# Kernel optimization log

Measured on AMD Instinct MI355X. Metric: run time of the kernel, lower is better.

The kernel has to match this reference:

```python
import jax, jax.numpy as jnp
import numpy as np
from jax import lax

# dims (see shape_source)
B, C, H, W = 2, 128, 48, 48
HEADS = 4
G = 4                 # offset_groups = heads
DH = C // HEADS       # 32, dim_head
DF = 4                # downsample_factor
OKS = 6               # offset_kernel_size
PAD = (OKS - DF) // 2 # 1
OFFSET_SCALE = 4.0
CPB_DIM = C // 4      # 32
OD = C // G           # offset_dims = 32


def setup_inputs() -> dict:
    key = jax.random.key(0)
    ks = jax.random.split(key, 12)
    rn = lambda k, shape, s=0.05: jax.random.normal(k, shape, dtype=jnp.float32) * s
    return {
        "x": jax.random.normal(ks[0], (B, C, H, W), dtype=jnp.float32),
        "gamma": jax.random.normal(ks[1], (1,), dtype=jnp.float32),  # nn.Parameter([0.0]); randomized so both paths contribute
        "wq": rn(ks[2], (G, DH, C // G)),    # grouped 1x1 conv, groups=G
        "wk": rn(ks[3], (G, DH, C // G)),
        "wv": rn(ks[4], (G, DH, C // G)),
        "wo": rn(ks[5], (C, C)),             # to_out 1x1 conv
        "bo": jnp.zeros((C,), jnp.float32),
        "w_off_dw": rn(ks[6], (OD, 1, OKS, OKS)),  # depthwise conv k=6 s=4 p=1
        "b_off_dw": jnp.zeros((OD,), jnp.float32),
        "w_off_proj": rn(ks[7], (2, OD)),          # 1x1 conv to 2 offset channels, no bias
        "cpb_w0": rn(ks[8], (2, CPB_DIM), 0.5),
        "cpb_b0": jnp.zeros((CPB_DIM,), jnp.float32),
        "cpb_w1": rn(ks[9], (CPB_DIM, CPB_DIM), 0.2),
        "cpb_b1": jnp.zeros((CPB_DIM,), jnp.float32),
        "cpb_w2": rn(ks[10], (CPB_DIM, HEADS // G), 0.2),
        "cpb_b2": jnp.zeros((HEADS // G,), jnp.float32),
    }


def _bilinear_sample(img, px, py):
    """F.grid_sample(mode='bilinear', padding_mode='zeros') on pixel coords.
    img: (N, Cg, Hi, Wi); px, py: (N, Ho, Wo) -> (N, Cg, Ho, Wo)"""
    N, Cg, Hi, Wi = img.shape
    imgf = img.reshape(N, Cg, Hi * Wi)
    x0 = jnp.floor(px)
    y0 = jnp.floor(py)
    wx1 = px - x0
    wy1 = py - y0

    def corner(xc, yc, w):
        valid = (xc >= 0) & (xc <= Wi - 1) & (yc >= 0) & (yc <= Hi - 1)
        xi = jnp.clip(xc, 0, Wi - 1).astype(jnp.int32)
        yi = jnp.clip(yc, 0, Hi - 1).astype(jnp.int32)
        idx = (yi * Wi + xi).reshape(N, -1)
        vals = jnp.take_along_axis(imgf, idx[:, None, :], axis=2)  # (N,Cg,Ho*Wo)
        return vals * (w * valid).reshape(N, 1, -1)

    out = (corner(x0, y0, (1 - wx1) * (1 - wy1))
           + corner(x0 + 1, y0, wx1 * (1 - wy1))
           + corner(x0, y0 + 1, (1 - wx1) * wy1)
           + corner(x0 + 1, y0 + 1, wx1 * wy1))
    return out.reshape(N, Cg, px.shape[1], px.shape[2])


def _forward(x, gamma, wq, wk, wv, wo, bo, w_off_dw, b_off_dw, w_off_proj,
             cpb_w0, cpb_b0, cpb_w1, cpb_b1, cpb_w2, cpb_b2):
    b = x.shape[0]
    scale = DH ** -0.5
    xg = x.reshape(b, G, C // G, H, W)
    # grouped 1x1 conv -> queries (b, G, DH, H, W); channel layout (g d) == (h d) since G==HEADS
    q = jnp.einsum('bgchw,goc->bgohw', xg, wq)
    gq = q.reshape(b * G, DH, H, W)
    # to_offsets: depthwise conv (k=6, s=4, p=1) -> GELU -> 1x1 to 2ch -> tanh -> *offset_scale
    off = lax.conv_general_dilated(gq, w_off_dw, (DF, DF), [(PAD, PAD), (PAD, PAD)],
                                   feature_group_count=OD,
                                   dimension_numbers=('NCHW', 'OIHW', 'NCHW'))
    off = jax.nn.gelu(off + b_off_dw[None, :, None, None], approximate=False)
    off = jnp.tanh(jnp.einsum('bchw,oc->bohw', off, w_off_proj)) * OFFSET_SCALE  # (bG,2,Hd,Wd)
    Hd, Wd = off.shape[-2], off.shape[-1]
    gy, gx = jnp.meshgrid(jnp.arange(Hd, dtype=jnp.float32),
                          jnp.arange(Wd, dtype=jnp.float32), indexing='ij')
    vg0 = gx[None] + off[:, 0]  # channel 0 = x (meshgrid 'xy' in torch code)
    vg1 = gy[None] + off[:, 1]  # channel 1 = y
    vn0 = 2.0 * vg0 / max(Hd - 1, 1) - 1.0  # normalize_grid (H==W so h/w quirk is moot)
    vn1 = 2.0 * vg1 / max(Wd - 1, 1) - 1.0
    # grid_sample align_corners=False unnormalization: pix = ((u+1)*size - 1)/2
    px = ((vn0 + 1.0) * W - 1.0) / 2.0
    py = ((vn1 + 1.0) * H - 1.0) / 2.0
    kv = _bilinear_sample(xg.reshape(b * G, C // G, H, W), px, py)  # (bG, C/G, Hd, Wd)
    kvg = kv.reshape(b, G, C // G, Hd, Wd)
    k = jnp.einsum('bgchw,goc->bgohw', kvg, wk)
    v = jnp.einsum('bgchw,goc->bgohw', kvg, wv)
    i, j = H * W, Hd * Wd
    qh = q.reshape(b, HEADS, DH, i).transpose(0, 1, 3, 2) * scale  # (b,h,i,d)
    kh = k.reshape(b, HEADS, DH, j).transpose(0, 1, 3, 2)
    vh = v.reshape(b, HEADS, DH, j).transpose(0, 1, 3, 2)
    sim = jnp.einsum('bhid,bhjd->bhij', qh, kh)
    # CPB relative position bias
    gyq, gxq = jnp.meshgrid(jnp.arange(H, dtype=jnp.float32),
                            jnp.arange(W, dtype=jnp.float32), indexing='ij')
    qn0 = 2.0 * gxq / max(H - 1, 1) - 1.0
    qn1 = 2.0 * gyq / max(W - 1, 1) - 1.0
    grid_q = jnp.stack([qn0, qn1], -1).reshape(1, i, 1, 2)
    grid_kv = jnp.stack([vn0, vn1], -1).reshape(b * G, 1, j, 2)
    pos = grid_q - grid_kv                       # (bG, i, j, 2)
    bias = jnp.sign(pos) * jnp.log1p(jnp.abs(pos))
    h1 = jax.nn.relu(bias @ cpb_w0 + cpb_b0)
    h2 = jax.nn.relu(h1 @ cpb_w1 + cpb_b1)
    bias = h2 @ cpb_w2 + cpb_b2                  # (bG, i, j, heads//G)
    bias = bias.reshape(b, G, i, j, HEADS // G).transpose(0, 1, 4, 2, 3).reshape(b, HEADS, i, j)
    attn = jax.nn.softmax(sim + bias, axis=-1)
    outh = jnp.einsum('bhij,bhjd->bhid', attn, vh)
    out = outh.transpose(0, 1, 3, 2).reshape(b, C, H, W)  # 'b h (x y) d -> b (h d) x y'
    attention = jnp.einsum('bchw,oc->bohw', out, wo) + bo[None, :, None, None]
    return gamma[0] * attention + x, attention


def reference(x, gamma, wq, wk, wv, wo, bo, w_off_dw, b_off_dw, w_off_proj,
              cpb_w0, cpb_b0, cpb_w1, cpb_b1, cpb_w2, cpb_b2):
    return _forward(x, gamma, wq, wk, wv, wo, bo, w_off_dw, b_off_dw, w_off_proj,
                    cpb_w0, cpb_b0, cpb_w1, cpb_b1, cpb_w2, cpb_b2)
```

## Files before the change

### kernel.cpp

```cpp
#include <hip/hip_runtime.h>
#include <math.h>

#define HWHW 2304
#define JD   144
#define LSP  148

typedef __attribute__((ext_vector_type(8))) short short8;
typedef __attribute__((ext_vector_type(4))) float f32x4;

__device__ inline ushort f2bf(float f) {
  uint u = __float_as_uint(f);
  u += 0x7fffu + ((u >> 16) & 1u);
  return (ushort)(u >> 16);
}
__device__ inline float bf2f(ushort s) { return __uint_as_float((uint)s << 16); }


__global__ __launch_bounds__(256) void qproj_kernel(
    const float* __restrict__ x, const float* __restrict__ wq,
    ushort* __restrict__ qt) {
  int hw = blockIdx.x * 256 + threadIdx.x;
  int o0 = blockIdx.y * 8, bg = blockIdx.z;
  int b = bg >> 2, g = bg & 3;
  const float* xp = x + (b * 128 + g * 32) * HWHW + hw;
  float xv[32];
#pragma unroll
  for (int c = 0; c < 32; ++c) xv[c] = xp[c * HWHW];
  uint p[4];
#pragma unroll
  for (int oo = 0; oo < 8; oo += 2) {
    const float* w0r = wq + (g * 32 + o0 + oo) * 32;
    const float* w1r = wq + (g * 32 + o0 + oo + 1) * 32;
    float a0 = 0.f, a1 = 0.f;
#pragma unroll
    for (int c = 0; c < 32; ++c) { a0 += w0r[c] * xv[c]; a1 += w1r[c] * xv[c]; }
    p[oo >> 1] = (uint)f2bf(a0) | ((uint)f2bf(a1) << 16);
  }
  *(uint4*)(qt + ((long)bg * HWHW + hw) * 32 + o0) = make_uint4(p[0], p[1], p[2], p[3]);
}

__global__ __launch_bounds__(384) void offset_kv_kernel(
    const ushort* __restrict__ qt, const float* __restrict__ wdw,
    const float* __restrict__ bdw, const float* __restrict__ wproj,
    const float* __restrict__ x, const float* __restrict__ wk,
    const float* __restrict__ wv,
    float* __restrict__ vn0, float* __restrict__ vn1,
    ushort* __restrict__ ktb, ushort* __restrict__ vtb) {
  __shared__ float qs[288][32];
  __shared__ float wdws[36][32];
  __shared__ float wkl[32][33], wvl[32][33];
  __shared__ float kvs[32][13];
  __shared__ float spx[12], spy[12];
  int hd = blockIdx.x, bg = blockIdx.y, b = bg >> 2, g = bg & 3;
  int t = threadIdx.x;
  for (int u = t; u < 9216; u += 384) {
    int r = u >> 5, c = u & 31;
    int ry = r / 48, col = r - ry * 48;
    int hy = hd * 4 - 1 + ry;
    float v = 0.f;
    if (hy >= 0 && hy < 48)
      v = bf2f(qt[((long)bg * HWHW + hy * 48 + col) * 32 + c]);
    qs[r][c] = v;
  }
  for (int u = t; u < 1152; u += 384) wdws[u >> 5][u & 31] = wdw[(u & 31) * 36 + (u >> 5)];
  for (int u = t; u < 1024; u += 384) {
    int d = u >> 5, c = u & 31;
    wkl[d][c] = wk[g * 1024 + u];
    wvl[d][c] = wv[g * 1024 + u];
  }
  __syncthreads();
  {
    int wd = t >> 5, c = t & 31;
    float s = 0.f;
#pragma unroll
    for (int ky = 0; ky < 6; ++ky) {
#pragma unroll
      for (int kx = 0; kx < 6; ++kx) {
        int wx = wd * 4 - 1 + kx;
        if (wx >= 0 && wx < 48)
          s += wdws[ky * 6 + kx][c] * qs[ky * 48 + wx][c];
      }
    }
    s += bdw[c];
    s = 0.5f * s * (1.f + erff(s * 0.70710678118654752f));
    float g0 = wproj[c] * s;
    float g1 = wproj[32 + c] * s;
#pragma unroll
    for (int k = 16; k >= 1; k >>= 1) {
      g0 += __shfl_xor(g0, k, 64);
      g1 += __shfl_xor(g1, k, 64);
    }
    if (c == 0) {
      float off0 = tanhf(g0) * 4.f;
      float off1 = tanhf(g1) * 4.f;
      float n0 = 2.f * ((float)wd + off0) / 11.f - 1.f;
      float n1 = 2.f * ((float)hd + off1) / 11.f - 1.f;
      int idx = bg * JD + hd * 12 + wd;
      vn0[idx] = n0;
      vn1[idx] = n1;
      spx[wd] = ((n0 + 1.f) * 48.f - 1.f) * 0.5f;
      spy[wd] = ((n1 + 1.f) * 48.f - 1.f) * 0.5f;
    }
  }
  __syncthreads();
  {
    int j = t >> 5, c = t & 31;
    float fx = spx[j], fy = spy[j];
    float x0 = floorf(fx), y0 = floorf(fy);
    float wx = fx - x0, wy = fy - y0;
    int xi = (int)x0, yi = (int)y0;
    const float* xp = x + (b * 128 + g * 32 + c) * HWHW;
    float v00 = 0.f, v10 = 0.f, v01 = 0.f, v11 = 0.f;
    bool okx0 = (xi >= 0) & (xi < 48), okx1 = (xi + 1 >= 0) & (xi + 1 < 48);
    if (yi >= 0 && yi < 48) {
      if (okx0) v00 = xp[yi * 48 + xi];
      if (okx1) v10 = xp[yi * 48 + xi + 1];
    }
    if (yi + 1 >= 0 && yi + 1 < 48) {
      if (okx0) v01 = xp[(yi + 1) * 48 + xi];
      if (okx1) v11 = xp[(yi + 1) * 48 + xi + 1];
    }
    kvs[c][j] = v00 * (1.f - wx) * (1.f - wy) + v10 * wx * (1.f - wy)
              + v01 * (1.f - wx) * wy + v11 * wx * wy;
  }
  __syncthreads();
  {
    int j = t >> 5, d = t & 31;
    float ak = 0.f, av = 0.f;
#pragma unroll
    for (int c = 0; c < 32; ++c) {
      float val = kvs[c][j];
      ak += wkl[d][c] * val;
      av += wvl[d][c] * val;
    }
    int jg = hd * 12 + j;
    ktb[bg * 4608 + jg * 32 + d] = f2bf(ak);
    vtb[bg * 5120 + d * 160 + jg] = f2bf(av);
  }
  if (hd == 0) {
    for (int u = t; u < 512; u += 384)
      vtb[bg * 5120 + (u >> 4) * 160 + 144 + (u & 15)] = 0;
  }
}

__global__ __launch_bounds__(256) void attn_fused_kernel(
    const ushort* __restrict__ qt, const ushort* __restrict__ ktb,
    const ushort* __restrict__ vtb,
    const float* __restrict__ vn0, const float* __restrict__ vn1,
    const float* __restrict__ w0, const float* __restrict__ b0,
    const float* __restrict__ w1, const float* __restrict__ b1,
    const float* __restrict__ w2, const float* __restrict__ b2,
    float* __restrict__ outh) {
  __shared__ __align__(16) char smem[21888];
  float* Ls = (float*)smem;
  ushort* kbf = (ushort*)(smem + 9472);
  ushort* vbfT = (ushort*)(smem + 9472);
  ushort* qbf = (ushort*)(smem + 19712);
  float* sv0 = (float*)(smem + 20736);
  float* sv1 = (float*)(smem + 21312);

  int bg = blockIdx.y, b = bg >> 2, g = bg & 3;
  int i0 = blockIdx.x * 16;
  int t = threadIdx.x;
  int w = t >> 6, lane = t & 63;
  int lam = lane & 15, quad = lane >> 4;

  {
    const uint* src = (const uint*)(ktb + bg * 4608);
    uint* dst = (uint*)kbf;
    for (int u = t; u < 2304; u += 256) dst[u] = src[u];
    ((uint*)qbf)[t] = ((const uint*)(qt + ((long)bg * HWHW + i0) * 32))[t];
  }
  if (t < JD) { sv0[t] = vn0[bg * JD + t]; sv1[t] = vn1[bg * JD + t]; }

  float w00r[8], w01r[8], b0r[8];
#pragma unroll
  for (int j = 0; j < 8; ++j) {
    int k = quad * 8 + j;
    w00r[j] = w0[k]; w01r[j] = w0[32 + k]; b0r[j] = b0[k];
  }
  short8 w1f0, w1f1;
#pragma unroll
  for (int j = 0; j < 8; ++j) {
    int k = quad * 8 + j;
    w1f0[j] = (short)f2bf(w1[k * 32 + lam]);
    w1f1[j] = (short)f2bf(w1[k * 32 + 16 + lam]);
  }
  f32x4 zA, zB;
  float w2r[8];
#pragma unroll
  for (int r = 0; r < 4; ++r) {
    zA[r] = b1[quad * 4 + r];
    zB[r] = b1[16 + quad * 4 + r];
    w2r[r] = w2[quad * 4 + r];
    w2r[4 + r] = w2[16 + quad * 4 + r];
  }
  float b2s = b2[0];

  __syncthreads();

  const float scale = 0.17677669529663687f;
  {
    short8 aq = *(const short8*)(qbf + lam * 32 + quad * 8);
#pragma unroll 1
    for (int jt = w; jt < 9; jt += 4) {
      short8 bk = *(const short8*)(kbf + (jt * 16 + lam) * 32 + quad * 8);
      f32x4 acc = {0.f, 0.f, 0.f, 0.f};
      acc = __builtin_amdgcn_mfma_f32_16x16x32_bf16(aq, bk, acc, 0, 0, 0);
#pragma unroll
      for (int r = 0; r < 4; ++r)
        Ls[(quad * 4 + r) * LSP + jt * 16 + lam] = acc[r] * scale;
    }
  }
  __syncthreads();

#pragma unroll 1
  for (int s = 0; s < 9; ++s) {
    int P = s * 64 + lane;
    int ii = P / 144, jj = P - ii * 144;
    int ig = i0 + w * 4 + ii;
    int iy = ig / 48, ix = ig - iy * 48;
    float p0 = (float)ix * (2.f / 47.f) - 1.f - sv0[jj];
    float p1 = (float)iy * (2.f / 47.f) - 1.f - sv1[jj];
    float s0f = copysignf(__logf(1.f + fabsf(p0)), p0);
    float s1f = copysignf(__logf(1.f + fabsf(p1)), p1);
    float bm[4];
#pragma unroll
    for (int mt = 0; mt < 4; ++mt) {
      float s0 = __shfl(s0f, mt * 16 + lam, 64);
      float s1 = __shfl(s1f, mt * 16 + lam, 64);
      float h[8];
#pragma unroll
      for (int j = 0; j < 8; ++j)
        h[j] = fmaxf(fmaf(s0, w00r[j], fmaf(s1, w01r[j], b0r[j])), 0.f);
      union { uint u[4]; short8 s8; } cvt;
#pragma unroll
      for (int j = 0; j < 4; ++j)
        cvt.u[j] = __builtin_amdgcn_perm(__float_as_uint(h[2 * j + 1]),
                                         __float_as_uint(h[2 * j]), 0x07060302);
      f32x4 dA = __builtin_amdgcn_mfma_f32_16x16x32_bf16(w1f0, cvt.s8, zA, 0, 0, 0);
      f32x4 dB = __builtin_amdgcn_mfma_f32_16x16x32_bf16(w1f1, cvt.s8, zB, 0, 0, 0);
      float acc = 0.f;
#pragma unroll
      for (int r = 0; r < 4; ++r) {
        acc = fmaf(fmaxf(dA[r], 0.f), w2r[r], acc);
        acc = fmaf(fmaxf(dB[r], 0.f), w2r[4 + r], acc);
      }
      acc += __shfl_xor(acc, 16, 64);
      acc += __shfl_xor(acc, 32, 64);
      bm[mt] = acc;
    }
    float biasv = (quad == 0 ? bm[0] : quad == 1 ? bm[1] : quad == 2 ? bm[2] : bm[3]) + b2s;
    Ls[(w * 4 + ii) * LSP + jj] += biasv;
  }
  __syncthreads();

  {
    const uint* src = (const uint*)(vtb + bg * 5120);
    uint* dst = (uint*)vbfT;
    for (int u = t; u < 2560; u += 256) dst[u] = src[u];
  }

#pragma unroll 1
  for (int rr = 0; rr < 4; ++rr) {
    int row = w * 4 + rr;
    const float* Lp = Ls + row * LSP;
    float l0 = Lp[lane], l1 = Lp[64 + lane];
    float l2 = (lane < 16) ? Lp[128 + lane] : -INFINITY;
    float m = fmaxf(fmaxf(l0, l1), l2);
#pragma unroll
    for (int k = 32; k >= 1; k >>= 1) m = fmaxf(m, __shfl_xor(m, k, 64));
    float e0 = __expf(l0 - m), e1 = __expf(l1 - m);
    float e2 = (lane < 16) ? __expf(l2 - m) : 0.f;
    float sum = e0 + e1 + e2;
#pragma unroll
    for (int k = 32; k >= 1; k >>= 1) sum += __shfl_xor(sum, k, 64);
    float inv = 1.f / sum;
    ushort* pb = (ushort*)(Lp + 64);
    pb[lane] = f2bf(e0 * inv);
    pb[64 + lane] = f2bf(e1 * inv);
    if (lane < 32) pb[128 + lane] = (lane < 16) ? f2bf(e2 * inv) : (ushort)0;
  }
  __syncthreads();

  if (w < 2) {
    f32x4 o = {0.f, 0.f, 0.f, 0.f};
    const ushort* pb = (const ushort*)(Ls + lam * LSP + 64);
    const ushort* vb = vbfT + (w * 16 + lam) * 160;
#pragma unroll
    for (int kb = 0; kb < 5; ++kb) {
      short8 ap = *(const short8*)(pb + kb * 32 + quad * 8);
      short8 bv = *(const short8*)(vb + kb * 32 + quad * 8);
      o = __builtin_amdgcn_mfma_f32_16x16x32_bf16(ap, bv, o, 0, 0, 0);
    }
#pragma unroll
    for (int r = 0; r < 4; ++r) {
      int ig = i0 + quad * 4 + r;
      outh[((long)b * HWHW + ig) * 128 + g * 32 + w * 16 + lam] = o[r];
    }
  }
}

__global__ __launch_bounds__(256) void out_kernel(
    const float* __restrict__ outh, const float* __restrict__ wo,
    const float* __restrict__ bo, const float* __restrict__ x,
    const float* __restrict__ gamma, float* __restrict__ out) {
  __shared__ float tile[64 * 129];
  int b = blockIdx.y;
  int hw0 = blockIdx.x * 64;
  int oc0 = blockIdx.z * 32;
  int t = threadIdx.x;
  int wid = t >> 6, lane = t & 63;
  for (int u = t; u < 2048; u += 256) {
    int r = u >> 5, c4 = (u & 31) * 4;
    const float4 v = *(const float4*)(outh + (b * HWHW + hw0 + r) * 128 + c4);
    float* dst = tile + r * 129 + c4;
    dst[0] = v.x; dst[1] = v.y; dst[2] = v.z; dst[3] = v.w;
  }
  __syncthreads();
  float acc[8];
#pragma unroll
  for (int o = 0; o < 8; ++o) acc[o] = 0.f;
  const float* wop = wo + (oc0 + wid * 8) * 128;
  const float* row = tile + lane * 129;
#pragma unroll 1
  for (int c4 = 0; c4 < 128; c4 += 4) {
    float v0 = row[c4], v1 = row[c4 + 1], v2 = row[c4 + 2], v3 = row[c4 + 3];
#pragma unroll
    for (int o = 0; o < 8; ++o) {
      acc[o] += wop[o * 128 + c4] * v0 + wop[o * 128 + c4 + 1] * v1
              + wop[o * 128 + c4 + 2] * v2 + wop[o * 128 + c4 + 3] * v3;
    }
  }
  float gm = gamma[0];
  float* out0 = out;
  float* out1 = out + 2 * 128 * HWHW;
#pragma unroll
  for (int o = 0; o < 8; ++o) {
    int oc = oc0 + wid * 8 + o;
    int idx = (b * 128 + oc) * HWHW + hw0 + lane;
    float a = acc[o] + bo[oc];
    out1[idx] = a;
    out0[idx] = fmaf(gm, a, x[idx]);
  }
}

extern "C" void kernel_launch(void* const* d_in, const int* in_sizes, int n_in,
                              void* d_out, int out_size, void* d_ws, size_t ws_size,
                              hipStream_t stream) {
  const float* x     = (const float*)d_in[0];
  const float* gamma = (const float*)d_in[1];
  const float* wq    = (const float*)d_in[2];
  const float* wk    = (const float*)d_in[3];
  const float* wv    = (const float*)d_in[4];
  const float* wo    = (const float*)d_in[5];
  const float* bo    = (const float*)d_in[6];
  const float* wdw   = (const float*)d_in[7];
  const float* bdw   = (const float*)d_in[8];
  const float* wproj = (const float*)d_in[9];
  const float* cw0   = (const float*)d_in[10];
  const float* cb0   = (const float*)d_in[11];
  const float* cw1   = (const float*)d_in[12];
  const float* cb1   = (const float*)d_in[13];
  const float* cw2   = (const float*)d_in[14];
  const float* cb2   = (const float*)d_in[15];
  char* wsb = (char*)d_ws;
  ushort* qt  = (ushort*)wsb;
  float* vn0  = (float*)(wsb + 1179648);
  float* vn1  = (float*)(wsb + 1184256);
  ushort* ktb = (ushort*)(wsb + 1188864);
  ushort* vtb = (ushort*)(wsb + 1262592);
  float* outh = (float*)(wsb + 1344512);
  float* out  = (float*)d_out;

  qproj_kernel<<<dim3(9, 4, 8), 256, 0, stream>>>(x, wq, qt);
  offset_kv_kernel<<<dim3(12, 8), 384, 0, stream>>>(qt, wdw, bdw, wproj, x, wk, wv,
                                                    vn0, vn1, ktb, vtb);
  attn_fused_kernel<<<dim3(144, 8), 256, 0, stream>>>(qt, ktb, vtb, vn0, vn1,
                                                      cw0, cb0, cw1, cb1, cw2, cb2, outh);
  out_kernel<<<dim3(36, 2, 4), 256, 0, stream>>>(outh, wo, bo, x, gamma, out);
}
```

Measured before the change: 153.1 us.

## Use bf16 MFMA for output projection and store attention output in bf16

```diff
diff --git a/kernel.cpp b/kernel.cpp
--- a/kernel.cpp
+++ b/kernel.cpp
@@ -53,14 +53,15 @@
   __shared__ float spx[12], spy[12];
   int hd = blockIdx.x, bg = blockIdx.y, b = bg >> 2, g = bg & 3;
   int t = threadIdx.x;
-  for (int u = t; u < 9216; u += 384) {
-    int r = u >> 5, c = u & 31;
+  for (int u = t; u < 4608; u += 384) {
+    int r = u >> 4, c2 = u & 15;
     int ry = r / 48, col = r - ry * 48;
     int hy = hd * 4 - 1 + ry;
-    float v = 0.f;
+    uint v = 0;
     if (hy >= 0 && hy < 48)
-      v = bf2f(qt[((long)bg * HWHW + hy * 48 + col) * 32 + c]);
-    qs[r][c] = v;
+      v = ((const uint*)qt)[((long)bg * HWHW + hy * 48 + col) * 16 + c2];
+    qs[r][c2 * 2] = bf2f((ushort)v);
+    qs[r][c2 * 2 + 1] = bf2f((ushort)(v >> 16));
   }
   for (int u = t; u < 1152; u += 384) wdws[u >> 5][u & 31] = wdw[(u & 31) * 36 + (u >> 5)];
   for (int u = t; u < 1024; u += 384) {
@@ -150,7 +151,7 @@
     const float* __restrict__ w0, const float* __restrict__ b0,
     const float* __restrict__ w1, const float* __restrict__ b1,
     const float* __restrict__ w2, const float* __restrict__ b2,
-    float* __restrict__ outh) {
+    ushort* __restrict__ outh) {
   __shared__ __align__(16) char smem[21888];
   float* Ls = (float*)smem;
   ushort* kbf = (ushort*)(smem + 9472);
@@ -166,10 +167,11 @@
   int lam = lane & 15, quad = lane >> 4;
 
   {
-    const uint* src = (const uint*)(ktb + bg * 4608);
-    uint* dst = (uint*)kbf;
-    for (int u = t; u < 2304; u += 256) dst[u] = src[u];
-    ((uint*)qbf)[t] = ((const uint*)(qt + ((long)bg * HWHW + i0) * 32))[t];
+    const uint4* src = (const uint4*)(ktb + bg * 4608);
+    uint4* dst = (uint4*)kbf;
+    for (int u = t; u < 576; u += 256) dst[u] = src[u];
+    if (t < 128) ((uint4*)qbf)[t & 127] =
+        ((const uint4*)(qt + ((long)bg * HWHW + i0) * 32))[t & 127];
   }
   if (t < JD) { sv0[t] = vn0[bg * JD + t]; sv1[t] = vn1[bg * JD + t]; }
 
@@ -256,9 +258,9 @@
   __syncthreads();
 
   {
-    const uint* src = (const uint*)(vtb + bg * 5120);
-    uint* dst = (uint*)vbfT;
-    for (int u = t; u < 2560; u += 256) dst[u] = src[u];
+    const uint4* src = (const uint4*)(vtb + bg * 5120);
+    uint4* dst = (uint4*)vbfT;
+    for (int u = t; u < 640; u += 256) dst[u] = src[u];
   }
 
 #pragma unroll 1
@@ -296,52 +298,61 @@
 #pragma unroll
     for (int r = 0; r < 4; ++r) {
       int ig = i0 + quad * 4 + r;
-      outh[((long)b * HWHW + ig) * 128 + g * 32 + w * 16 + lam] = o[r];
+      outh[((long)b * HWHW + ig) * 128 + g * 32 + w * 16 + lam] = f2bf(o[r]);
     }
   }
 }
 
 __global__ __launch_bounds__(256) void out_kernel(
-    const float* __restrict__ outh, const float* __restrict__ wo,
+    const ushort* __restrict__ outh, const float* __restrict__ wo,
     const float* __restrict__ bo, const float* __restrict__ x,
     const float* __restrict__ gamma, float* __restrict__ out) {
-  __shared__ float tile[64 * 129];
+  __shared__ __align__(16) char smem[39168];
+  ushort* wob = (ushort*)smem;
+  ushort* aob = (ushort*)(smem + 34816);
   int b = blockIdx.y;
-  int hw0 = blockIdx.x * 64;
-  int oc0 = blockIdx.z * 32;
+  int hw0 = blockIdx.x * 16;
   int t = threadIdx.x;
-  int wid = t >> 6, lane = t & 63;
-  for (int u = t; u < 2048; u += 256) {
-    int r = u >> 5, c4 = (u & 31) * 4;
-    const float4 v = *(const float4*)(outh + (b * HWHW + hw0 + r) * 128 + c4);
-    float* dst = tile + r * 129 + c4;
-    dst[0] = v.x; dst[1] = v.y; dst[2] = v.z; dst[3] = v.w;
-  }
-  __syncthreads();
-  float acc[8];
-#pragma unroll
-  for (int o = 0; o < 8; ++o) acc[o] = 0.f;
-  const float* wop = wo + (oc0 + wid * 8) * 128;
-  const float* row = tile + lane * 129;
-#pragma unroll 1
-  for (int c4 = 0; c4 < 128; c4 += 4) {
-    float v0 = row[c4], v1 = row[c4 + 1], v2 = row[c4 + 2], v3 = row[c4 + 3];
-#pragma unroll
-    for (int o = 0; o < 8; ++o) {
-      acc[o] += wop[o * 128 + c4] * v0 + wop[o * 128 + c4 + 1] * v1
-              + wop[o * 128 + c4 + 2] * v2 + wop[o * 128 + c4 + 3] * v3;
-    }
+  int w = t >> 6, lane = t & 63, lam = lane & 15, quad = lane >> 4;
+  {
+    const float2* wsrc = (const float2*)wo;
+    for (int u = t; u < 8192; u += 256) {
+      float2 v = wsrc[u];
+      ((uint*)wob)[(u >> 6) * 68 + (u & 63)] =
+          (uint)f2bf(v.x) | ((uint)f2bf(v.y) << 16);
+    }
+  }
+  {
+    const uint* src = (const uint*)(outh + ((long)b * HWHW + hw0) * 128);
+    for (int u = t; u < 1024; u += 256)
+      ((uint*)aob)[(u >> 6) * 68 + (u & 63)] = src[u];
+  }
+  __syncthreads();
+  f32x4 acc0 = {0.f, 0.f, 0.f, 0.f}, acc1 = {0.f, 0.f, 0.f, 0.f};
+#pragma unroll
+  for (int ks = 0; ks < 4; ++ks) {
+    short8 a = *(const short8*)(aob + lam * 136 + ks * 32 + quad * 8);
+    short8 b0f = *(const short8*)(wob + (w * 32 + lam) * 136 + ks * 32 + quad * 8);
+    short8 b1f = *(const short8*)(wob + (w * 32 + 16 + lam) * 136 + ks * 32 + quad * 8);
+    acc0 = __builtin_amdgcn_mfma_f32_16x16x32_bf16(a, b0f, acc0, 0, 0, 0);
+    acc1 = __builtin_amdgcn_mfma_f32_16x16x32_bf16(a, b1f, acc1, 0, 0, 0);
   }
   float gm = gamma[0];
   float* out0 = out;
   float* out1 = out + 2 * 128 * HWHW;
 #pragma unroll
-  for (int o = 0; o < 8; ++o) {
-    int oc = oc0 + wid * 8 + o;
-    int idx = (b * 128 + oc) * HWHW + hw0 + lane;
-    float a = acc[o] + bo[oc];
-    out1[idx] = a;
-    out0[idx] = fmaf(gm, a, x[idx]);
+  for (int nt = 0; nt < 2; ++nt) {
+    f32x4 acc = nt ? acc1 : acc0;
+    int oc = w * 32 + nt * 16 + lam;
+    float bv = bo[oc];
+    long base = ((long)(b * 128 + oc)) * HWHW + hw0 + quad * 4;
+    float4 xv = *(const float4*)(x + base);
+    float4 a1, a0;
+    a1.x = acc[0] + bv; a1.y = acc[1] + bv; a1.z = acc[2] + bv; a1.w = acc[3] + bv;
+    a0.x = fmaf(gm, a1.x, xv.x); a0.y = fmaf(gm, a1.y, xv.y);
+    a0.z = fmaf(gm, a1.z, xv.z); a0.w = fmaf(gm, a1.w, xv.w);
+    *(float4*)(out1 + base) = a1;
+    *(float4*)(out0 + base) = a0;
   }
 }
 
@@ -370,7 +381,7 @@
   float* vn1  = (float*)(wsb + 1184256);
   ushort* ktb = (ushort*)(wsb + 1188864);
   ushort* vtb = (ushort*)(wsb + 1262592);
-  float* outh = (float*)(wsb + 1344512);
+  ushort* outh = (ushort*)(wsb + 1344512);
   float* out  = (float*)d_out;
 
   qproj_kernel<<<dim3(9, 4, 8), 256, 0, stream>>>(x, wq, qt);
@@ -378,5 +389,5 @@
                                                     vn0, vn1, ktb, vtb);
   attn_fused_kernel<<<dim3(144, 8), 256, 0, stream>>>(qt, ktb, vtb, vn0, vn1,
                                                       cw0, cb0, cw1, cb1, cw2, cb2, outh);
-  out_kernel<<<dim3(36, 2, 4), 256, 0, stream>>>(outh, wo, bo, x, gamma, out);
-}
+  out_kernel<<<dim3(144, 2), 256, 0, stream>>>(outh, wo, bo, x, gamma, out);
+}
```

After: 138.0 us. 1.11x faster.
